# Kernel tuning notes

Measured on AMD Instinct MI355X. Metric: run time of the kernel, lower is better.

The kernel has to match this reference:

```python
import jax, jax.numpy as jnp
import numpy as np

N_NODES = 100000
N_EDGES = 1600000
N_GRAPHS = 256
D_IN = 128
D_HID = 128
D_OUT = 64


def graph_conv(x, src, dst, W_rel, b_rel, W_root):
    # PyG GraphConv: out = lin_rel(mean_{j->i} x_j) + lin_root(x)
    msgs = jax.ops.segment_sum(x[src], dst, num_segments=N_NODES)  # [N, d]
    deg = jax.ops.segment_sum(jnp.ones((src.shape[0],), x.dtype), dst, num_segments=N_NODES)
    agg = msgs / jnp.maximum(deg, 1.0)[:, None]
    return agg @ W_rel + b_rel + x @ W_root


def setup_inputs() -> dict:
    key = jax.random.key(0)
    ks = jax.random.split(key, 12)
    x = jax.random.normal(ks[0], (N_NODES, D_IN), dtype=jnp.float32)
    edge_index = jax.random.randint(ks[1], (2, N_EDGES), 0, N_NODES, dtype=jnp.int64)
    batch = jnp.sort(jax.random.randint(ks[2], (N_NODES,), 0, N_GRAPHS, dtype=jnp.int64))
    def lin(k, fan_in, fan_out):
        bound = 1.0 / np.sqrt(fan_in)
        return jax.random.uniform(k, (fan_in, fan_out), jnp.float32, -bound, bound)
    inp = {
        "x": x, "edge_index": edge_index, "batch": batch,
        "W1_rel": lin(ks[3], D_IN, D_HID), "b1_rel": jnp.zeros((D_HID,), jnp.float32), "W1_root": lin(ks[4], D_IN, D_HID),
        "W2_rel": lin(ks[5], D_HID, D_HID), "b2_rel": jnp.zeros((D_HID,), jnp.float32), "W2_root": lin(ks[6], D_HID, D_HID),
        "W3_rel": lin(ks[7], D_HID, D_HID), "b3_rel": jnp.zeros((D_HID,), jnp.float32), "W3_root": lin(ks[8], D_HID, D_HID),
        "Wl": lin(ks[9], D_HID, D_OUT), "bl": jnp.zeros((D_OUT,), jnp.float32),
    }
    return inp


def reference(x, edge_index, batch, W1_rel, b1_rel, W1_root, W2_rel, b2_rel, W2_root,
              W3_rel, b3_rel, W3_root, Wl, bl):
    src, dst = edge_index[0], edge_index[1]
    h = jax.nn.relu(graph_conv(x, src, dst, W1_rel, b1_rel, W1_root))
    h = jax.nn.relu(graph_conv(h, src, dst, W2_rel, b2_rel, W2_root))
    h = graph_conv(h, src, dst, W3_rel, b3_rel, W3_root)
    # global mean pool over graphs
    sums = jax.ops.segment_sum(h, batch, num_segments=N_GRAPHS)          # [G, d]
    cnts = jax.ops.segment_sum(jnp.ones((h.shape[0],), h.dtype), batch, num_segments=N_GRAPHS)
    pooled = sums / jnp.maximum(cnts, 1.0)[:, None]
    # dropout is identity at inference
    return pooled @ Wl + bl  # [G, D_OUT]
```

## Files before the change

### kernel.cpp

```cpp
#include <hip/hip_runtime.h>
#include <hip/hip_bf16.h>

#define N_NODES  100000
#define N_EDGES  1600000
#define N_GRAPHS 256
#define DCH      128
#define DOUT     64
#define NB       391
#define PADB     512
#define SLACK    4608
#define CHUNK    2048
#define NBINA    782

typedef short v8s __attribute__((ext_vector_type(8)));
typedef float v4f __attribute__((ext_vector_type(4)));

static __device__ __forceinline__ float bf2f(unsigned short u) {
    unsigned int x = ((unsigned int)u) << 16;
    return __builtin_bit_cast(float, x);
}
static __device__ __forceinline__ unsigned short f2bf(float f) {
    unsigned int x = __builtin_bit_cast(unsigned int, f);
    unsigned int r = (x + 0x7fffu + ((x >> 16) & 1u)) >> 16;
    return (unsigned short)r;
}
static __device__ __forceinline__ int clampi(int v, int lo, int hi) {
    return v < lo ? lo : (v > hi ? hi : v);
}

__global__ void __launch_bounds__(256) binAprep_kernel(
    const int* __restrict__ src, const int* __restrict__ dst,
    int* __restrict__ gcur, uint2* __restrict__ region,
    const float* __restrict__ x, unsigned short* __restrict__ B2,
    const float* __restrict__ W1rel, const float* __restrict__ W1root,
    const float* __restrict__ W2rel, const float* __restrict__ W2root,
    const float* __restrict__ W3rel, const float* __restrict__ W3root,
    unsigned short* __restrict__ frag,
    unsigned short* __restrict__ z1, unsigned short* __restrict__ z2)
{
    __shared__ uint2 stage[CHUNK];
    __shared__ int hcnt[PADB], hcnt2[PADB], hoff[PADB], garr[PADB];
    __shared__ int s2[256];
    int tid = threadIdx.x;

    if (blockIdx.x >= NBINA) {
        int bid = blockIdx.x - NBINA;
        if (bid < 12500) {
            size_t i = ((size_t)bid * 256 + tid) * 4;
            float4 f = *reinterpret_cast<const float4*>(x + i);
            uint2 o;
            o.x = ((unsigned)f2bf(f.y) << 16) | (unsigned)f2bf(f.x);
            o.y = ((unsigned)f2bf(f.w) << 16) | (unsigned)f2bf(f.z);
            *reinterpret_cast<uint2*>(B2 + i) = o;
        } else if (bid < 12548) {
            int gid = (bid - 12500) * 256 + tid;
            int lane = gid & 63;
            int nt   = (gid >> 6) & 7;
            int kt   = (gid >> 9) & 7;
            int L    = gid >> 12;
            const float* rel  = (L == 0) ? W1rel  : (L == 1) ? W2rel  : W3rel;
            const float* root = (L == 0) ? W1root : (L == 1) ? W2root : W3root;
            int n  = nt * 16 + (lane & 15);
            int k0 = kt * 32 + (lane >> 4) * 8;
            unsigned short o[8];
            #pragma unroll
            for (int j = 0; j < 8; j++) {
                int k = k0 + j;
                float w = (k < 128) ? rel[k * 128 + n] : root[(k - 128) * 128 + n];
                o[j] = f2bf(w);
            }
            uint4 u;
            u.x = (unsigned)o[0] | ((unsigned)o[1] << 16);
            u.y = (unsigned)o[2] | ((unsigned)o[3] << 16);
            u.z = (unsigned)o[4] | ((unsigned)o[5] << 16);
            u.w = (unsigned)o[6] | ((unsigned)o[7] << 16);
            *reinterpret_cast<uint4*>(frag + (size_t)gid * 8) = u;
        } else {
            if (tid < 64)       reinterpret_cast<unsigned*>(z1)[tid] = 0;
            else if (tid < 128) reinterpret_cast<unsigned*>(z2)[tid - 64] = 0;
        }
        return;
    }

    int e0  = blockIdx.x * CHUNK;
    int nedge = N_EDGES - e0; if (nedge > CHUNK) nedge = CHUNK;

    for (int b = tid; b < PADB; b += 256) { hcnt[b] = 0; hcnt2[b] = 0; }
    __syncthreads();

    int es[CHUNK / 256], ed[CHUNK / 256];
    #pragma unroll
    for (int j = 0; j < CHUNK / 256; j++) {
        int e = e0 + j * 256 + tid;
        if (e < N_EDGES) {
            es[j] = clampi(src[e], 0, N_NODES - 1);
            ed[j] = clampi(dst[e], 0, N_NODES - 1);
            atomicAdd(&hcnt[ed[j] >> 8], 1);
        } else { es[j] = -1; ed[j] = 0; }
    }
    __syncthreads();

    int v0 = hcnt[2 * tid], v1 = hcnt[2 * tid + 1];
    s2[tid] = v0 + v1; __syncthreads();
    for (int off = 1; off < 256; off <<= 1) {
        int xx = (tid >= off) ? s2[tid - off] : 0;
        __syncthreads();
        s2[tid] += xx;
        __syncthreads();
    }
    int excl = s2[tid] - (v0 + v1);
    hoff[2 * tid] = excl; hoff[2 * tid + 1] = excl + v0;
    __syncthreads();

    for (int b = tid; b < NB; b += 256) {
        int c = hcnt[b];
        garr[b] = b * SLACK + ((c > 0) ? atomicAdd(&gcur[b], c) : 0);
    }
    __syncthreads();

    #pragma unroll
    for (int j = 0; j < CHUNK / 256; j++) {
        if (es[j] >= 0) {
            int b = ed[j] >> 8;
            int pos = atomicAdd(&hcnt2[b], 1) + hoff[b];
            stage[pos] = (uint2){(unsigned)es[j], (unsigned)ed[j]};
        }
    }
    __syncthreads();

    for (int i = tid; i < nedge; i += 256) {
        uint2 en = stage[i];
        int b = (int)(en.y >> 8);
        int gpos = garr[b] + (i - hoff[b]);
        if (gpos < (b + 1) * SLACK) region[gpos] = en;
    }
}

__global__ void __launch_bounds__(256) binFinish_kernel(const uint2* __restrict__ region, const int* __restrict__ gcur,
                                                        int* __restrict__ rowptr, int* __restrict__ csr) {
    __shared__ int h[256], sc[256], cur[256], s2[256], hoff[PADB];
    int b = blockIdx.x, tid = threadIdx.x;
    int c0 = gcur[2 * tid];     if (c0 > SLACK) c0 = SLACK;
    int c1 = gcur[2 * tid + 1]; if (c1 > SLACK) c1 = SLACK;
    s2[tid] = c0 + c1;
    h[tid] = 0;
    __syncthreads();
    for (int off = 1; off < 256; off <<= 1) {
        int xx = (tid >= off) ? s2[tid - off] : 0;
        __syncthreads();
        s2[tid] += xx;
        __syncthreads();
    }
    int excl = s2[tid] - (c0 + c1);
    hoff[2 * tid] = excl; hoff[2 * tid + 1] = excl + c0;
    __syncthreads();
    if (b == 0 && tid == 255) rowptr[N_NODES] = s2[255];
    int base = hoff[b];
    int size = gcur[b]; if (size > SLACK) size = SLACK;
    int node0 = b * 256;
    for (int j = tid; j < size; j += 256) {
        unsigned loc = region[b * SLACK + j].y - (unsigned)node0;
        if (loc < 256u) atomicAdd(&h[loc], 1);
    }
    __syncthreads();
    int v = h[tid]; sc[tid] = v; __syncthreads();
    for (int off = 1; off < 256; off <<= 1) {
        int xx = (tid >= off) ? sc[tid - off] : 0;
        __syncthreads();
        sc[tid] += xx;
        __syncthreads();
    }
    int myptr = base + sc[tid] - v;
    int node = node0 + tid;
    if (node < N_NODES) rowptr[node] = myptr;
    cur[tid] = myptr;
    __syncthreads();
    for (int j = tid; j < size; j += 256) {
        uint2 en = region[b * SLACK + j];
        unsigned loc = en.y - (unsigned)node0;
        if (loc < 256u) {
            int p = atomicAdd(&cur[loc], 1);
            if (p >= 0 && p < N_EDGES) csr[p] = (int)en.x;
        }
    }
}

__global__ void __launch_bounds__(256, 6) layer_kernel(
    const unsigned short* __restrict__ hin,
    const int* __restrict__ rowptr, const int* __restrict__ csr,
    const unsigned short* __restrict__ frag, const float* __restrict__ bias,
    unsigned short* __restrict__ hout,
    const int* __restrict__ batch, float* __restrict__ psum, int mode)
{
    __shared__ __attribute__((aligned(16))) unsigned short As[16 * DCH];
    const int wave = threadIdx.x >> 6;
    const int lane = threadIdx.x & 63;
    const int l16  = lane & 15;
    const int quad = lane >> 4;
    const int base = blockIdx.x * 16;
    char* Asb = reinterpret_cast<char*>(As);

    #pragma unroll
    for (int k = 0; k < 4; k++) {
        const int row  = wave * 4 + k;
        const int node = base + row;
        const int r0 = rowptr[node];
        const int r1 = rowptr[node + 1];
        float a0 = 0.f, a1 = 0.f;
        int t = csr[r0 + l16];
        for (int c = r0; c < r1; c += 16) {
            int tn = csr[c + 16 + l16];
            int idx = (c + l16 < r1) ? t : N_NODES;
            #pragma unroll
            for (int j = 0; j < 16; j++) {
                int s = __builtin_amdgcn_readlane(idx, j);
                unsigned v = *reinterpret_cast<const unsigned*>(hin + (size_t)s * DCH + lane * 2);
                a0 += bf2f((unsigned short)(v & 0xffffu));
                a1 += bf2f((unsigned short)(v >> 16));
            }
            t = tn;
        }
        int deg = r1 - r0;
        float inv = 1.0f / (float)(deg > 1 ? deg : 1);
        unsigned o = ((unsigned)f2bf(a1 * inv) << 16) | (unsigned)f2bf(a0 * inv);
        *reinterpret_cast<unsigned*>(Asb + row * 256 + ((lane * 4) ^ ((row & 7) << 4))) = o;
    }
    __syncthreads();

    const int nt0 = wave * 2;
    v4f acc0 = (v4f){0.f, 0.f, 0.f, 0.f};
    v4f acc1 = (v4f){0.f, 0.f, 0.f, 0.f};
    #pragma unroll
    for (int kt = 0; kt < 8; kt++) {
        v8s av;
        if (kt < 4) {
            int co = (kt * 64 + quad * 16) ^ ((l16 & 7) << 4);
            av = *reinterpret_cast<const v8s*>(Asb + l16 * 256 + co);
        } else {
            int ak = (kt - 4) * 32 + quad * 8;
            av = *reinterpret_cast<const v8s*>(hin + (size_t)(base + l16) * DCH + ak);
        }
        v8s b0 = *reinterpret_cast<const v8s*>(frag + (((size_t)(kt * 8 + nt0)) * 64 + lane) * 8);
        v8s b1 = *reinterpret_cast<const v8s*>(frag + (((size_t)(kt * 8 + nt0 + 1)) * 64 + lane) * 8);
        acc0 = __builtin_amdgcn_mfma_f32_16x16x32_bf16(av, b0, acc0, 0, 0, 0);
        acc1 = __builtin_amdgcn_mfma_f32_16x16x32_bf16(av, b1, acc1, 0, 0, 0);
    }

    const int n0 = nt0 * 16 + l16;
    const int n1 = n0 + 16;
    const float bv0 = bias[n0];
    const float bv1 = bias[n1];

    if (mode != 2) {
        #pragma unroll
        for (int r = 0; r < 4; r++) {
            int row = base + quad * 4 + r;
            float x0 = acc0[r] + bv0;
            float x1 = acc1[r] + bv1;
            if (mode == 1) { x0 = fmaxf(x0, 0.f); x1 = fmaxf(x1, 0.f); }
            hout[(size_t)row * DCH + n0] = f2bf(x0);
            hout[(size_t)row * DCH + n1] = f2bf(x1);
        }
    } else {
        bool fast = (batch[base] == batch[base + 15]);
        if (fast) {
            int g = batch[base];
            float s0 = acc0[0] + acc0[1] + acc0[2] + acc0[3] + 4.0f * bv0;
            float s1 = acc1[0] + acc1[1] + acc1[2] + acc1[3] + 4.0f * bv1;
            s0 += __shfl_xor(s0, 16); s0 += __shfl_xor(s0, 32);
            s1 += __shfl_xor(s1, 16); s1 += __shfl_xor(s1, 32);
            if (quad == 0) {
                atomicAdd(&psum[g * DCH + n0], s0);
                atomicAdd(&psum[g * DCH + n1], s1);
            }
        } else {
            int g[4];
            #pragma unroll
            for (int r = 0; r < 4; r++) g[r] = batch[base + quad * 4 + r];
            float s0 = 0.f, s1 = 0.f; int cg = -1;
            #pragma unroll
            for (int r = 0; r < 4; r++) {
                if (g[r] != cg) {
                    if (cg >= 0) {
                        atomicAdd(&psum[cg * DCH + n0], s0);
                        atomicAdd(&psum[cg * DCH + n1], s1);
                    }
                    s0 = 0.f; s1 = 0.f; cg = g[r];
                }
                s0 += acc0[r] + bv0;
                s1 += acc1[r] + bv1;
            }
            if (cg >= 0) {
                atomicAdd(&psum[cg * DCH + n0], s0);
                atomicAdd(&psum[cg * DCH + n1], s1);
            }
        }
    }
}

static __device__ __forceinline__ int lowerb(const int* __restrict__ a, int n, int key) {
    int lo = 0, hi = n;
    while (lo < hi) { int mid = (lo + hi) >> 1; if (a[mid] < key) lo = mid + 1; else hi = mid; }
    return lo;
}

__global__ void __launch_bounds__(64) final_kernel(const float* __restrict__ psum,
                                                   const int* __restrict__ batch,
                                                   const float* __restrict__ Wl, const float* __restrict__ bl,
                                                   float* __restrict__ out) {
    __shared__ float ps[DCH];
    __shared__ int bounds[2];
    int g = blockIdx.x, tid = threadIdx.x;
    if (tid == 0) {
        bounds[0] = lowerb(batch, N_NODES, g);
        bounds[1] = lowerb(batch, N_NODES, g + 1);
    }
    __syncthreads();
    int cnt = bounds[1] - bounds[0];
    float inv = 1.0f / (float)(cnt > 1 ? cnt : 1);
    ps[tid] = psum[g * DCH + tid] * inv;
    ps[tid + 64] = psum[g * DCH + tid + 64] * inv;
    __syncthreads();
    float o = 0.f;
    #pragma unroll 4
    for (int c = 0; c < DCH; c++) o += ps[c] * Wl[c * DOUT + tid];
    out[g * DOUT + tid] = o + bl[tid];
}

extern "C" void kernel_launch(void* const* d_in, const int* in_sizes, int n_in,
                              void* d_out, int out_size, void* d_ws, size_t ws_size,
                              hipStream_t stream) {
    const float* x     = (const float*)d_in[0];
    const int*   edge  = (const int*)d_in[1];
    const int*   src   = edge;
    const int*   dst   = edge + N_EDGES;
    const int*   batch = (const int*)d_in[2];
    const float* W1rel  = (const float*)d_in[3];
    const float* b1     = (const float*)d_in[4];
    const float* W1root = (const float*)d_in[5];
    const float* W2rel  = (const float*)d_in[6];
    const float* b2     = (const float*)d_in[7];
    const float* W2root = (const float*)d_in[8];
    const float* W3rel  = (const float*)d_in[9];
    const float* b3     = (const float*)d_in[10];
    const float* W3root = (const float*)d_in[11];
    const float* Wl     = (const float*)d_in[12];
    const float* bl     = (const float*)d_in[13];
    float* out = (float*)d_out;

    char* ws = (char*)d_ws;
    size_t off = 0;
    auto carve = [&](size_t bytes) -> void* {
        void* p = ws + off;
        off += (bytes + 255) & ~(size_t)255;
        return p;
    };
    int*            rowptr  = (int*)carve((size_t)(N_NODES + 1) * 4);
    int*            csr     = (int*)carve((size_t)(N_EDGES + 64) * 4);
    int*            gcur    = (int*)carve((size_t)PADB * 4 + (size_t)N_GRAPHS * DCH * 4);
    float*          psum    = (float*)(gcur + PADB);
    unsigned short* frag    = (unsigned short*)carve((size_t)3 * 8 * 8 * 64 * 8 * 2);
    unsigned short* B1      = (unsigned short*)carve((size_t)(N_NODES + 1) * DCH * 2);
    unsigned short* B2      = (unsigned short*)carve((size_t)(N_NODES + 1) * DCH * 2);
    uint2*          region  = (uint2*)B1;

    hipMemsetAsync(gcur, 0, (size_t)PADB * 4 + (size_t)N_GRAPHS * DCH * 4, stream);

    binAprep_kernel<<<NBINA + 12549, 256, 0, stream>>>(src, dst, gcur, region,
                                                       x, B2, W1rel, W1root, W2rel, W2root, W3rel, W3root,
                                                       frag, B1 + (size_t)N_NODES * DCH, B2 + (size_t)N_NODES * DCH);
    binFinish_kernel<<<NB, 256, 0, stream>>>(region, gcur, rowptr, csr);

    const int layerGrid = N_NODES / 16;

    layer_kernel<<<layerGrid, 256, 0, stream>>>(B2, rowptr, csr, frag,         b1, B1, batch, psum, 1);
    layer_kernel<<<layerGrid, 256, 0, stream>>>(B1, rowptr, csr, frag + 32768, b2, B2, batch, psum, 1);
    layer_kernel<<<layerGrid, 256, 0, stream>>>(B2, rowptr, csr, frag + 65536, b3, B1, batch, psum, 2);

    final_kernel<<<N_GRAPHS, 64, 0, stream>>>(psum, batch, Wl, bl, out);
}
```

Before: 387.6 us.

## Replace two-pass binned CSR build with degree-count, scan, atomic scatter

Replaces the bucketed staging approach (per-chunk LDS sort into slack regions, then a per-bucket finish pass) with a classic CSR build. A degree kernel runs global atomics per edge, a scan kernel computes rowptr and cursors, and a scatter kernel places src ids via per-destination global atomics. The x-to-bf16 conversion and weight-fragment prep are merged into the scatter kernel. This removes the intermediate region buffer and its extra read/write pass, but adds 1.6M contended global atomics twice and uncoalesced scattered csr writes, and the within-row edge order becomes nondeterministic.

```diff
diff --git a/kernel.cpp b/kernel.cpp
--- a/kernel.cpp
+++ b/kernel.cpp
@@ -6,11 +6,9 @@
 #define N_GRAPHS 256
 #define DCH      128
 #define DOUT     64
-#define NB       391
+#define NBK      391
+#define DEGPAD   100096
 #define PADB     512
-#define SLACK    4608
-#define CHUNK    2048
-#define NBINA    782
 
 typedef short v8s __attribute__((ext_vector_type(8)));
 typedef float v4f __attribute__((ext_vector_type(4)));
@@ -28,9 +26,65 @@
     return v < lo ? lo : (v > hi ? hi : v);
 }
 
-__global__ void __launch_bounds__(256) binAprep_kernel(
+__global__ void __launch_bounds__(256) deg_kernel(const int* __restrict__ dst,
+                                                  int* __restrict__ deg, int* __restrict__ bsum) {
+    __shared__ int hcnt[PADB];
+    int tid = threadIdx.x;
+    int e0  = blockIdx.x * 2048;
+    for (int b = tid; b < PADB; b += 256) hcnt[b] = 0;
+    __syncthreads();
+    #pragma unroll
+    for (int j = 0; j < 8; j++) {
+        int e = e0 + j * 256 + tid;
+        if (e < N_EDGES) {
+            int d = clampi(dst[e], 0, N_NODES - 1);
+            atomicAdd(&deg[d], 1);
+            atomicAdd(&hcnt[d >> 8], 1);
+        }
+    }
+    __syncthreads();
+    for (int b = tid; b < PADB; b += 256) {
+        int c = hcnt[b];
+        if (c > 0) atomicAdd(&bsum[b], c);
+    }
+}
+
+__global__ void __launch_bounds__(256) rowcur_kernel(const int* __restrict__ bsum, const int* __restrict__ deg,
+                                                     int* __restrict__ rowptr, int* __restrict__ cur) {
+    __shared__ int s2[256], sc[256], hoff[PADB];
+    int b = blockIdx.x, tid = threadIdx.x;
+    int c0 = bsum[2 * tid], c1 = bsum[2 * tid + 1];
+    s2[tid] = c0 + c1;
+    __syncthreads();
+    for (int off = 1; off < 256; off <<= 1) {
+        int xx = (tid >= off) ? s2[tid - off] : 0;
+        __syncthreads();
+        s2[tid] += xx;
+        __syncthreads();
+    }
+    int excl = s2[tid] - (c0 + c1);
+    hoff[2 * tid] = excl; hoff[2 * tid + 1] = excl + c0;
+    __syncthreads();
+    if (b == 0 && tid == 255) rowptr[N_NODES] = s2[255];
+    int base = hoff[b];
+    int node = b * 256 + tid;
+    int d = deg[node];
+    sc[tid] = d;
+    __syncthreads();
+    for (int off = 1; off < 256; off <<= 1) {
+        int xx = (tid >= off) ? sc[tid - off] : 0;
+        __syncthreads();
+        sc[tid] += xx;
+        __syncthreads();
+    }
+    int myptr = base + sc[tid] - d;
+    if (node < N_NODES) rowptr[node] = myptr;
+    cur[node] = myptr;
+}
+
+__global__ void __launch_bounds__(256) scatPrep_kernel(
     const int* __restrict__ src, const int* __restrict__ dst,
-    int* __restrict__ gcur, uint2* __restrict__ region,
+    int* __restrict__ cur, int* __restrict__ csr,
     const float* __restrict__ x, unsigned short* __restrict__ B2,
     const float* __restrict__ W1rel, const float* __restrict__ W1root,
     const float* __restrict__ W2rel, const float* __restrict__ W2root,
@@ -38,150 +92,55 @@
     unsigned short* __restrict__ frag,
     unsigned short* __restrict__ z1, unsigned short* __restrict__ z2)
 {
-    __shared__ uint2 stage[CHUNK];
-    __shared__ int hcnt[PADB], hcnt2[PADB], hoff[PADB], garr[PADB];
-    __shared__ int s2[256];
     int tid = threadIdx.x;
-
-    if (blockIdx.x >= NBINA) {
-        int bid = blockIdx.x - NBINA;
-        if (bid < 12500) {
-            size_t i = ((size_t)bid * 256 + tid) * 4;
-            float4 f = *reinterpret_cast<const float4*>(x + i);
-            uint2 o;
-            o.x = ((unsigned)f2bf(f.y) << 16) | (unsigned)f2bf(f.x);
-            o.y = ((unsigned)f2bf(f.w) << 16) | (unsigned)f2bf(f.z);
-            *reinterpret_cast<uint2*>(B2 + i) = o;
-        } else if (bid < 12548) {
-            int gid = (bid - 12500) * 256 + tid;
-            int lane = gid & 63;
-            int nt   = (gid >> 6) & 7;
-            int kt   = (gid >> 9) & 7;
-            int L    = gid >> 12;
-            const float* rel  = (L == 0) ? W1rel  : (L == 1) ? W2rel  : W3rel;
-            const float* root = (L == 0) ? W1root : (L == 1) ? W2root : W3root;
-            int n  = nt * 16 + (lane & 15);
-            int k0 = kt * 32 + (lane >> 4) * 8;
-            unsigned short o[8];
-            #pragma unroll
-            for (int j = 0; j < 8; j++) {
-                int k = k0 + j;
-                float w = (k < 128) ? rel[k * 128 + n] : root[(k - 128) * 128 + n];
-                o[j] = f2bf(w);
-            }
-            uint4 u;
-            u.x = (unsigned)o[0] | ((unsigned)o[1] << 16);
-            u.y = (unsigned)o[2] | ((unsigned)o[3] << 16);
-            u.z = (unsigned)o[4] | ((unsigned)o[5] << 16);
-            u.w = (unsigned)o[6] | ((unsigned)o[7] << 16);
-            *reinterpret_cast<uint4*>(frag + (size_t)gid * 8) = u;
-        } else {
-            if (tid < 64)       reinterpret_cast<unsigned*>(z1)[tid] = 0;
-            else if (tid < 128) reinterpret_cast<unsigned*>(z2)[tid - 64] = 0;
+    if (blockIdx.x < 1563) {
+        int e0 = blockIdx.x * 1024;
+        #pragma unroll
+        for (int j = 0; j < 4; j++) {
+            int e = e0 + j * 256 + tid;
+            if (e < N_EDGES) {
+                int d = clampi(dst[e], 0, N_NODES - 1);
+                int s = clampi(src[e], 0, N_NODES - 1);
+                int p = atomicAdd(&cur[d], 1);
+                csr[p] = s;
+            }
         }
         return;
     }
-
-    int e0  = blockIdx.x * CHUNK;
-    int nedge = N_EDGES - e0; if (nedge > CHUNK) nedge = CHUNK;
-
-    for (int b = tid; b < PADB; b += 256) { hcnt[b] = 0; hcnt2[b] = 0; }
-    __syncthreads();
-
-    int es[CHUNK / 256], ed[CHUNK / 256];
-    #pragma unroll
-    for (int j = 0; j < CHUNK / 256; j++) {
-        int e = e0 + j * 256 + tid;
-        if (e < N_EDGES) {
-            es[j] = clampi(src[e], 0, N_NODES - 1);
-            ed[j] = clampi(dst[e], 0, N_NODES - 1);
-            atomicAdd(&hcnt[ed[j] >> 8], 1);
-        } else { es[j] = -1; ed[j] = 0; }
-    }
-    __syncthreads();
-
-    int v0 = hcnt[2 * tid], v1 = hcnt[2 * tid + 1];
-    s2[tid] = v0 + v1; __syncthreads();
-    for (int off = 1; off < 256; off <<= 1) {
-        int xx = (tid >= off) ? s2[tid - off] : 0;
-        __syncthreads();
-        s2[tid] += xx;
-        __syncthreads();
-    }
-    int excl = s2[tid] - (v0 + v1);
-    hoff[2 * tid] = excl; hoff[2 * tid + 1] = excl + v0;
-    __syncthreads();
-
-    for (int b = tid; b < NB; b += 256) {
-        int c = hcnt[b];
-        garr[b] = b * SLACK + ((c > 0) ? atomicAdd(&gcur[b], c) : 0);
-    }
-    __syncthreads();
-
-    #pragma unroll
-    for (int j = 0; j < CHUNK / 256; j++) {
-        if (es[j] >= 0) {
-            int b = ed[j] >> 8;
-            int pos = atomicAdd(&hcnt2[b], 1) + hoff[b];
-            stage[pos] = (uint2){(unsigned)es[j], (unsigned)ed[j]};
-        }
-    }
-    __syncthreads();
-
-    for (int i = tid; i < nedge; i += 256) {
-        uint2 en = stage[i];
-        int b = (int)(en.y >> 8);
-        int gpos = garr[b] + (i - hoff[b]);
-        if (gpos < (b + 1) * SLACK) region[gpos] = en;
-    }
-}
-
-__global__ void __launch_bounds__(256) binFinish_kernel(const uint2* __restrict__ region, const int* __restrict__ gcur,
-                                                        int* __restrict__ rowptr, int* __restrict__ csr) {
-    __shared__ int h[256], sc[256], cur[256], s2[256], hoff[PADB];
-    int b = blockIdx.x, tid = threadIdx.x;
-    int c0 = gcur[2 * tid];     if (c0 > SLACK) c0 = SLACK;
-    int c1 = gcur[2 * tid + 1]; if (c1 > SLACK) c1 = SLACK;
-    s2[tid] = c0 + c1;
-    h[tid] = 0;
-    __syncthreads();
-    for (int off = 1; off < 256; off <<= 1) {
-        int xx = (tid >= off) ? s2[tid - off] : 0;
-        __syncthreads();
-        s2[tid] += xx;
-        __syncthreads();
-    }
-    int excl = s2[tid] - (c0 + c1);
-    hoff[2 * tid] = excl; hoff[2 * tid + 1] = excl + c0;
-    __syncthreads();
-    if (b == 0 && tid == 255) rowptr[N_NODES] = s2[255];
-    int base = hoff[b];
-    int size = gcur[b]; if (size > SLACK) size = SLACK;
-    int node0 = b * 256;
-    for (int j = tid; j < size; j += 256) {
-        unsigned loc = region[b * SLACK + j].y - (unsigned)node0;
-        if (loc < 256u) atomicAdd(&h[loc], 1);
-    }
-    __syncthreads();
-    int v = h[tid]; sc[tid] = v; __syncthreads();
-    for (int off = 1; off < 256; off <<= 1) {
-        int xx = (tid >= off) ? sc[tid - off] : 0;
-        __syncthreads();
-        sc[tid] += xx;
-        __syncthreads();
-    }
-    int myptr = base + sc[tid] - v;
-    int node = node0 + tid;
-    if (node < N_NODES) rowptr[node] = myptr;
-    cur[tid] = myptr;
-    __syncthreads();
-    for (int j = tid; j < size; j += 256) {
-        uint2 en = region[b * SLACK + j];
-        unsigned loc = en.y - (unsigned)node0;
-        if (loc < 256u) {
-            int p = atomicAdd(&cur[loc], 1);
-            if (p >= 0 && p < N_EDGES) csr[p] = (int)en.x;
-        }
+    int bid = blockIdx.x - 1563;
+    if (bid < 12500) {
+        size_t i = ((size_t)bid * 256 + tid) * 4;
+        float4 f = *reinterpret_cast<const float4*>(x + i);
+        uint2 o;
+        o.x = ((unsigned)f2bf(f.y) << 16) | (unsigned)f2bf(f.x);
+        o.y = ((unsigned)f2bf(f.w) << 16) | (unsigned)f2bf(f.z);
+        *reinterpret_cast<uint2*>(B2 + i) = o;
+    } else if (bid < 12548) {
+        int gid = (bid - 12500) * 256 + tid;
+        int lane = gid & 63;
+        int nt   = (gid >> 6) & 7;
+        int kt   = (gid >> 9) & 7;
+        int L    = gid >> 12;
+        const float* rel  = (L == 0) ? W1rel  : (L == 1) ? W2rel  : W3rel;
+        const float* root = (L == 0) ? W1root : (L == 1) ? W2root : W3root;
+        int n  = nt * 16 + (lane & 15);
+        int k0 = kt * 32 + (lane >> 4) * 8;
+        unsigned short o[8];
+        #pragma unroll
+        for (int j = 0; j < 8; j++) {
+            int k = k0 + j;
+            float w = (k < 128) ? rel[k * 128 + n] : root[(k - 128) * 128 + n];
+            o[j] = f2bf(w);
+        }
+        uint4 u;
+        u.x = (unsigned)o[0] | ((unsigned)o[1] << 16);
+        u.y = (unsigned)o[2] | ((unsigned)o[3] << 16);
+        u.z = (unsigned)o[4] | ((unsigned)o[5] << 16);
+        u.w = (unsigned)o[6] | ((unsigned)o[7] << 16);
+        *reinterpret_cast<uint4*>(frag + (size_t)gid * 8) = u;
+    } else {
+        if (tid < 64)       reinterpret_cast<unsigned*>(z1)[tid] = 0;
+        else if (tid < 128) reinterpret_cast<unsigned*>(z2)[tid - 64] = 0;
     }
 }
 
@@ -357,19 +316,22 @@
     };
     int*            rowptr  = (int*)carve((size_t)(N_NODES + 1) * 4);
     int*            csr     = (int*)carve((size_t)(N_EDGES + 64) * 4);
-    int*            gcur    = (int*)carve((size_t)PADB * 4 + (size_t)N_GRAPHS * DCH * 4);
-    float*          psum    = (float*)(gcur + PADB);
+    int*            meta    = (int*)carve((size_t)DEGPAD * 4 + (size_t)PADB * 4 + (size_t)N_GRAPHS * DCH * 4);
+    int*            deg     = meta;
+    int*            bsum    = meta + DEGPAD;
+    float*          psum    = (float*)(meta + DEGPAD + PADB);
+    int*            cur     = (int*)carve((size_t)DEGPAD * 4);
     unsigned short* frag    = (unsigned short*)carve((size_t)3 * 8 * 8 * 64 * 8 * 2);
     unsigned short* B1      = (unsigned short*)carve((size_t)(N_NODES + 1) * DCH * 2);
     unsigned short* B2      = (unsigned short*)carve((size_t)(N_NODES + 1) * DCH * 2);
-    uint2*          region  = (uint2*)B1;
-
-    hipMemsetAsync(gcur, 0, (size_t)PADB * 4 + (size_t)N_GRAPHS * DCH * 4, stream);
-
-    binAprep_kernel<<<NBINA + 12549, 256, 0, stream>>>(src, dst, gcur, region,
-                                                       x, B2, W1rel, W1root, W2rel, W2root, W3rel, W3root,
-                                                       frag, B1 + (size_t)N_NODES * DCH, B2 + (size_t)N_NODES * DCH);
-    binFinish_kernel<<<NB, 256, 0, stream>>>(region, gcur, rowptr, csr);
+
+    hipMemsetAsync(meta, 0, (size_t)DEGPAD * 4 + (size_t)PADB * 4 + (size_t)N_GRAPHS * DCH * 4, stream);
+
+    deg_kernel<<<782, 256, 0, stream>>>(dst, deg, bsum);
+    rowcur_kernel<<<NBK, 256, 0, stream>>>(bsum, deg, rowptr, cur);
+    scatPrep_kernel<<<1563 + 12549, 256, 0, stream>>>(src, dst, cur, csr,
+                                                      x, B2, W1rel, W1root, W2rel, W2root, W3rel, W3root,
+                                                      frag, B1 + (size_t)N_NODES * DCH, B2 + (size_t)N_NODES * DCH);
 
     const int layerGrid = N_NODES / 16;
 
```

After: 557.3 us. 1.44x slower.

## Pack binned edges into 32-bit words and move prep work into finish kernel

Applied to the files above, without the earlier changes.

Binned edges are now stored as a single 32-bit word holding the source index shifted left by 8 with the low 8 bits of the destination, instead of an 8-byte pair. This halves region write and read traffic between the binning and CSR-finish passes. The x-to-bf16 conversion and weight fragment prep move from the binning kernel into the finish kernel's extra blocks, so they overlap with CSR finishing rather than with binning. The packing relies on node indices fitting in 24 bits, which holds for 100k nodes.

```diff
diff --git a/kernel.cpp b/kernel.cpp
--- a/kernel.cpp
+++ b/kernel.cpp
@@ -28,9 +28,70 @@
     return v < lo ? lo : (v > hi ? hi : v);
 }
 
-__global__ void __launch_bounds__(256) binAprep_kernel(
-    const int* __restrict__ src, const int* __restrict__ dst,
-    int* __restrict__ gcur, uint2* __restrict__ region,
+__global__ void __launch_bounds__(256) binA_kernel(const int* __restrict__ src, const int* __restrict__ dst,
+                                                   int* __restrict__ gcur, unsigned* __restrict__ region) {
+    __shared__ uint2 stage[CHUNK];
+    __shared__ int hcnt[PADB], hcnt2[PADB], hoff[PADB], garr[PADB];
+    __shared__ int s2[256];
+    int tid = threadIdx.x;
+    int e0  = blockIdx.x * CHUNK;
+    int nedge = N_EDGES - e0; if (nedge > CHUNK) nedge = CHUNK;
+
+    for (int b = tid; b < PADB; b += 256) { hcnt[b] = 0; hcnt2[b] = 0; }
+    __syncthreads();
+
+    int es[CHUNK / 256], ed[CHUNK / 256];
+    #pragma unroll
+    for (int j = 0; j < CHUNK / 256; j++) {
+        int e = e0 + j * 256 + tid;
+        if (e < N_EDGES) {
+            es[j] = clampi(src[e], 0, N_NODES - 1);
+            ed[j] = clampi(dst[e], 0, N_NODES - 1);
+            atomicAdd(&hcnt[ed[j] >> 8], 1);
+        } else { es[j] = -1; ed[j] = 0; }
+    }
+    __syncthreads();
+
+    int v0 = hcnt[2 * tid], v1 = hcnt[2 * tid + 1];
+    s2[tid] = v0 + v1; __syncthreads();
+    for (int off = 1; off < 256; off <<= 1) {
+        int xx = (tid >= off) ? s2[tid - off] : 0;
+        __syncthreads();
+        s2[tid] += xx;
+        __syncthreads();
+    }
+    int excl = s2[tid] - (v0 + v1);
+    hoff[2 * tid] = excl; hoff[2 * tid + 1] = excl + v0;
+    __syncthreads();
+
+    for (int b = tid; b < NB; b += 256) {
+        int c = hcnt[b];
+        garr[b] = b * SLACK + ((c > 0) ? atomicAdd(&gcur[b], c) : 0);
+    }
+    __syncthreads();
+
+    #pragma unroll
+    for (int j = 0; j < CHUNK / 256; j++) {
+        if (es[j] >= 0) {
+            int b = ed[j] >> 8;
+            int pos = atomicAdd(&hcnt2[b], 1) + hoff[b];
+            stage[pos] = (uint2){(unsigned)es[j], (unsigned)ed[j]};
+        }
+    }
+    __syncthreads();
+
+    for (int i = tid; i < nedge; i += 256) {
+        uint2 en = stage[i];
+        int b = (int)(en.y >> 8);
+        int gpos = garr[b] + (i - hoff[b]);
+        if (gpos < (b + 1) * SLACK)
+            region[gpos] = (en.x << 8) | (en.y & 255u);
+    }
+}
+
+__global__ void __launch_bounds__(256) binFinishPrep_kernel(
+    const unsigned* __restrict__ region, const int* __restrict__ gcur,
+    int* __restrict__ rowptr, int* __restrict__ csr,
     const float* __restrict__ x, unsigned short* __restrict__ B2,
     const float* __restrict__ W1rel, const float* __restrict__ W1root,
     const float* __restrict__ W2rel, const float* __restrict__ W2root,
@@ -38,13 +99,11 @@
     unsigned short* __restrict__ frag,
     unsigned short* __restrict__ z1, unsigned short* __restrict__ z2)
 {
-    __shared__ uint2 stage[CHUNK];
-    __shared__ int hcnt[PADB], hcnt2[PADB], hoff[PADB], garr[PADB];
-    __shared__ int s2[256];
+    __shared__ int h[256], sc[256], cur[256], s2[256], hoff[PADB];
     int tid = threadIdx.x;
 
-    if (blockIdx.x >= NBINA) {
-        int bid = blockIdx.x - NBINA;
+    if (blockIdx.x >= NB) {
+        int bid = blockIdx.x - NB;
         if (bid < 12500) {
             size_t i = ((size_t)bid * 256 + tid) * 4;
             float4 f = *reinterpret_cast<const float4*>(x + i);
@@ -82,64 +141,7 @@
         return;
     }
 
-    int e0  = blockIdx.x * CHUNK;
-    int nedge = N_EDGES - e0; if (nedge > CHUNK) nedge = CHUNK;
-
-    for (int b = tid; b < PADB; b += 256) { hcnt[b] = 0; hcnt2[b] = 0; }
-    __syncthreads();
-
-    int es[CHUNK / 256], ed[CHUNK / 256];
-    #pragma unroll
-    for (int j = 0; j < CHUNK / 256; j++) {
-        int e = e0 + j * 256 + tid;
-        if (e < N_EDGES) {
-            es[j] = clampi(src[e], 0, N_NODES - 1);
-            ed[j] = clampi(dst[e], 0, N_NODES - 1);
-            atomicAdd(&hcnt[ed[j] >> 8], 1);
-        } else { es[j] = -1; ed[j] = 0; }
-    }
-    __syncthreads();
-
-    int v0 = hcnt[2 * tid], v1 = hcnt[2 * tid + 1];
-    s2[tid] = v0 + v1; __syncthreads();
-    for (int off = 1; off < 256; off <<= 1) {
-        int xx = (tid >= off) ? s2[tid - off] : 0;
-        __syncthreads();
-        s2[tid] += xx;
-        __syncthreads();
-    }
-    int excl = s2[tid] - (v0 + v1);
-    hoff[2 * tid] = excl; hoff[2 * tid + 1] = excl + v0;
-    __syncthreads();
-
-    for (int b = tid; b < NB; b += 256) {
-        int c = hcnt[b];
-        garr[b] = b * SLACK + ((c > 0) ? atomicAdd(&gcur[b], c) : 0);
-    }
-    __syncthreads();
-
-    #pragma unroll
-    for (int j = 0; j < CHUNK / 256; j++) {
-        if (es[j] >= 0) {
-            int b = ed[j] >> 8;
-            int pos = atomicAdd(&hcnt2[b], 1) + hoff[b];
-            stage[pos] = (uint2){(unsigned)es[j], (unsigned)ed[j]};
-        }
-    }
-    __syncthreads();
-
-    for (int i = tid; i < nedge; i += 256) {
-        uint2 en = stage[i];
-        int b = (int)(en.y >> 8);
-        int gpos = garr[b] + (i - hoff[b]);
-        if (gpos < (b + 1) * SLACK) region[gpos] = en;
-    }
-}
-
-__global__ void __launch_bounds__(256) binFinish_kernel(const uint2* __restrict__ region, const int* __restrict__ gcur,
-                                                        int* __restrict__ rowptr, int* __restrict__ csr) {
-    __shared__ int h[256], sc[256], cur[256], s2[256], hoff[PADB];
-    int b = blockIdx.x, tid = threadIdx.x;
+    int b = blockIdx.x;
     int c0 = gcur[2 * tid];     if (c0 > SLACK) c0 = SLACK;
     int c1 = gcur[2 * tid + 1]; if (c1 > SLACK) c1 = SLACK;
     s2[tid] = c0 + c1;
@@ -159,8 +161,8 @@
     int size = gcur[b]; if (size > SLACK) size = SLACK;
     int node0 = b * 256;
     for (int j = tid; j < size; j += 256) {
-        unsigned loc = region[b * SLACK + j].y - (unsigned)node0;
-        if (loc < 256u) atomicAdd(&h[loc], 1);
+        unsigned loc = region[b * SLACK + j] & 255u;
+        atomicAdd(&h[loc], 1);
     }
     __syncthreads();
     int v = h[tid]; sc[tid] = v; __syncthreads();
@@ -176,12 +178,10 @@
     cur[tid] = myptr;
     __syncthreads();
     for (int j = tid; j < size; j += 256) {
-        uint2 en = region[b * SLACK + j];
-        unsigned loc = en.y - (unsigned)node0;
-        if (loc < 256u) {
-            int p = atomicAdd(&cur[loc], 1);
-            if (p >= 0 && p < N_EDGES) csr[p] = (int)en.x;
-        }
+        unsigned en = region[b * SLACK + j];
+        unsigned loc = en & 255u;
+        int p = atomicAdd(&cur[loc], 1);
+        if (p >= 0 && p < N_EDGES) csr[p] = (int)(en >> 8);
     }
 }
 
@@ -362,14 +362,14 @@
     unsigned short* frag    = (unsigned short*)carve((size_t)3 * 8 * 8 * 64 * 8 * 2);
     unsigned short* B1      = (unsigned short*)carve((size_t)(N_NODES + 1) * DCH * 2);
     unsigned short* B2      = (unsigned short*)carve((size_t)(N_NODES + 1) * DCH * 2);
-    uint2*          region  = (uint2*)B1;
+    unsigned*       region  = (unsigned*)B1;
 
     hipMemsetAsync(gcur, 0, (size_t)PADB * 4 + (size_t)N_GRAPHS * DCH * 4, stream);
 
-    binAprep_kernel<<<NBINA + 12549, 256, 0, stream>>>(src, dst, gcur, region,
-                                                       x, B2, W1rel, W1root, W2rel, W2root, W3rel, W3root,
-                                                       frag, B1 + (size_t)N_NODES * DCH, B2 + (size_t)N_NODES * DCH);
-    binFinish_kernel<<<NB, 256, 0, stream>>>(region, gcur, rowptr, csr);
+    binA_kernel<<<NBINA, 256, 0, stream>>>(src, dst, gcur, region);
+    binFinishPrep_kernel<<<NB + 12549, 256, 0, stream>>>(region, gcur, rowptr, csr,
+                                                         x, B2, W1rel, W1root, W2rel, W2root, W3rel, W3root,
+                                                         frag, B1 + (size_t)N_NODES * DCH, B2 + (size_t)N_NODES * DCH);
 
     const int layerGrid = N_NODES / 16;
 
```

Result: no change. 381.5 us (-1.6%).
